# Kernel optimization log

Hardware: AMD Instinct MI355X
Metric: run time of the kernel (lower is better)

Reference implementation:

```python
import jax, jax.numpy as jnp
import numpy as np

NEG_SLOPE = 0.2
EPS = 1e-16


def gat_layer(x, src, dst, W, att, bias, heads, out_ch, concat, num_nodes, edge_weight):
    """WeightedGATConv forward (eval mode, dropout off).
    x: [N, Fin], src/dst: [E], W: [Fin, H*C], att: [H, 2C], bias: [H*C] or [C].
    """
    H, C = heads, out_ch
    xp = (x @ W).reshape(-1, H, C)           # [N, H, C]
    xi = xp[dst]                              # target features  [E, H, C]
    xj = xp[src]                              # source features  [E, H, C]
    # attention logits: (cat(xi, xj) * att).sum(-1)
    alpha = jnp.einsum('ehc,hc->eh', xi, att[:, :C]) + jnp.einsum('ehc,hc->eh', xj, att[:, C:])
    alpha = jnp.where(alpha >= 0, alpha, NEG_SLOPE * alpha)   # leaky_relu
    # segment softmax over incoming edges of each destination node
    amax = jax.ops.segment_max(alpha, dst, num_segments=num_nodes)  # [N, H]
    amax = jnp.where(jnp.isfinite(amax), amax, 0.0)
    ex = jnp.exp(alpha - amax[dst])                                  # [E, H]
    denom = jax.ops.segment_sum(ex, dst, num_segments=num_nodes)     # [N, H]
    a = ex / (denom[dst] + EPS)                                      # [E, H]
    msg = xj * a[..., None]                                          # [E, H, C]
    if edge_weight is not None:
        msg = msg * edge_weight[:, None, None]
    out = jax.ops.segment_sum(msg, dst, num_segments=num_nodes)      # [N, H, C]
    out = out.reshape(num_nodes, H * C) if concat else out.mean(axis=1)
    return out + bias


def setup_inputs() -> dict:
    key = jax.random.key(0)
    ks = jax.random.split(key, 10)
    N, E = 20000, 320000
    IN, HID, LAT, H = 512, 256, 128, 4
    C1 = HID // H
    glorot = lambda k, shp: jax.random.uniform(k, shp, jnp.float32, -1.0, 1.0) * jnp.sqrt(6.0 / (shp[-2] + shp[-1]))
    return {
        'x': jax.random.normal(ks[0], (N, IN), jnp.float32),
        'edge_index': jax.random.randint(ks[1], (2, E), 0, N, jnp.int32),
        'edge_weight': jax.random.uniform(ks[2], (E,), jnp.float32),
        'W1': glorot(ks[3], (IN, H * C1)),
        'att1': glorot(ks[4], (H, 2 * C1)),
        'b1': jnp.zeros((H * C1,), jnp.float32),
        'Wmu': glorot(ks[5], (HID, LAT)),
        'attmu': glorot(ks[6], (1, 2 * LAT)),
        'bmu': jnp.zeros((LAT,), jnp.float32),
        'Wlv': glorot(ks[7], (HID, LAT)),
        'attlv': glorot(ks[8], (1, 2 * LAT)),
        'blv': jnp.zeros((LAT,), jnp.float32),
    }


def reference(x, edge_index, edge_weight, W1, att1, b1, Wmu, attmu, bmu, Wlv, attlv, blv):
    N = x.shape[0]
    src, dst = edge_index[0], edge_index[1]
    H = att1.shape[0]
    C1 = att1.shape[1] // 2
    LAT = Wmu.shape[1]
    h = gat_layer(x, src, dst, W1, att1, b1, H, C1, True, N, edge_weight)
    h = jax.nn.elu(h)
    mu = gat_layer(h, src, dst, Wmu, attmu, bmu, 1, LAT, False, N, edge_weight)
    logvar = gat_layer(h, src, dst, Wlv, attlv, blv, 1, LAT, False, N, edge_weight)
    return (mu, logvar)
```

## Files before the change

kernel.cpp:

```cpp
#include <hip/hip_runtime.h>
#include <stdint.h>

#define NEG_SLOPE 0.2f
#define SEPS 1e-16f

typedef short bf16x8 __attribute__((ext_vector_type(8)));
typedef float f32x4 __attribute__((ext_vector_type(4)));

static __device__ __forceinline__ float bf2f(ushort u) {
  union { uint32_t i; float f; } v; v.i = ((uint32_t)u) << 16; return v.f;
}
static __device__ __forceinline__ ushort f2bf(float f) {
  uint32_t b = __float_as_uint(f);
  b += 0x7FFFu + ((b >> 16) & 1u);
  return (ushort)(b >> 16);
}
static __device__ __forceinline__ float blo(uint32_t u) { return __uint_as_float(u << 16); }
static __device__ __forceinline__ float bhi(uint32_t u) { return __uint_as_float(u & 0xFFFF0000u); }
static __device__ __forceinline__ float ldf(const void* p, size_t i, int mode) {
  return mode ? ((const float*)p)[i] : bf2f(((const ushort*)p)[i]);
}

__global__ void fill_out(float* __restrict__ out, int n, float v) {
  int i = blockIdx.x * 256 + threadIdx.x;
  if (i < n) out[i] = v;
}
__global__ void fill_i32(int* __restrict__ p, int n, int v) {
  int i = blockIdx.x * 256 + threadIdx.x;
  if (i < n) p[i] = v;
}

struct DetPtrs {
  const uint32_t* p[11];
  int n[11];
  const uint32_t* idx;
  int idxn;
};
__global__ void detect_all(DetPtrs dp, int* __restrict__ modes) {
  int b = blockIdx.x;
  __shared__ int sL, sH;
  if (threadIdx.x == 0) { sL = 0; sH = 0; }
  __syncthreads();
  if (b < 11) {
    const uint32_t* w = dp.p[b];
    int elems = dp.n[b];
    int nprobe = min(2048, elems / 2);
    int cL = 0, cH = 0;
    for (int i = threadIdx.x; i < nprobe; i += 256) {
      uint32_t v = w[i];
      uint32_t eL = (v >> 7) & 0xFFu;
      uint32_t eH = (v >> 23) & 0xFFu;
      if (eL >= 90u && eL <= 128u) cL++;
      if (eH >= 90u && eH <= 128u) cH++;
    }
    atomicAdd(&sL, cL); atomicAdd(&sH, cH);
    __syncthreads();
    if (threadIdx.x == 0) {
      int m;
      if (sL * 4 >= nprobe * 3) m = 0;
      else if (sH * 4 >= nprobe) m = 1;
      else m = 0;
      modes[b] = m;
    }
  } else {
    const uint32_t* w = dp.idx;
    int nprobe = min(4096, dp.idxn);
    int c = 0;
    for (int i = threadIdx.x; i < nprobe; i += 256)
      if ((i & 1) && w[i] == 0u) c++;
    atomicAdd(&sL, c);
    __syncthreads();
    if (threadIdx.x == 0) modes[11] = (sL * 4 >= (nprobe / 2) * 3) ? 1 : 0;
  }
}

__global__ void canon_edges(const void* __restrict__ ei, const void* __restrict__ ew,
                            int* __restrict__ srcc, int* __restrict__ dstc,
                            int* __restrict__ deg, float* __restrict__ ewf,
                            int E, int N, const int* __restrict__ modes) {
  int i = blockIdx.x * 256 + threadIdx.x;
  if (i >= E) return;
  int s, d;
  if (modes[11]) {
    s = (int)((const long long*)ei)[i];
    d = (int)((const long long*)ei)[E + i];
  } else {
    s = ((const int*)ei)[i];
    d = ((const int*)ei)[E + i];
  }
  s = min(max(s, 0), N - 1);
  d = min(max(d, 0), N - 1);
  srcc[i] = s;
  dstc[i] = d;
  atomicAdd(&deg[d], 1);
  float v = ldf(ew, i, modes[1]);
  if (!isfinite(v)) v = 0.f;
  ewf[i] = v;
}

struct WTArgs {
  const void* w1; const void* wmu; const void* wlv;
  ushort* wt1; ushort* wall;
};
__global__ void canon_wt(WTArgs a, const int* __restrict__ modes) {
  int i = blockIdx.x * 256 + threadIdx.x;
  const int NW1 = 256 * 512;
  if (i < NW1) {
    int n = i >> 9, k = i & 511;
    float v = ldf(a.w1, (size_t)k * 256 + n, modes[2]);
    if (!isfinite(v)) v = 0.f;
    a.wt1[i] = f2bf(v);
  } else {
    int j = i - NW1;
    if (j >= 256 * 256) return;
    int n = j >> 8, k = j & 255;
    float v;
    if (n < 128) v = ldf(a.wmu, (size_t)k * 128 + n, modes[5]);
    else         v = ldf(a.wlv, (size_t)k * 128 + (n - 128), modes[8]);
    if (!isfinite(v)) v = 0.f;
    a.wall[j] = f2bf(v);
  }
}
struct SmallCan { const void* src[6]; float* dst[6]; int n[6]; int mi[6]; };
__global__ void canon_small(SmallCan a, const int* __restrict__ modes) {
  int b = blockIdx.x;
  int m = modes[a.mi[b]];
  const void* s = a.src[b];
  float* d = a.dst[b];
  for (int i = threadIdx.x; i < a.n[b]; i += 256) {
    float v = ldf(s, i, m);
    if (!isfinite(v)) v = 0.f;
    d[i] = v;
  }
}

__global__ __launch_bounds__(1024) void scan_deg(const int* __restrict__ deg,
                                                 int* __restrict__ row_ptr,
                                                 int* __restrict__ row_cur, int N) {
  __shared__ int part[1024];
  int t = threadIdx.x;
  int chunk = (N + 1023) / 1024;
  int lo = t * chunk, hi = min(lo + chunk, N);
  int s = 0;
  for (int i = lo; i < hi; ++i) s += deg[i];
  part[t] = s;
  __syncthreads();
  for (int off = 1; off < 1024; off <<= 1) {
    int v = (t >= off) ? part[t - off] : 0;
    __syncthreads();
    part[t] += v;
    __syncthreads();
  }
  int base = (t == 0) ? 0 : part[t - 1];
  for (int i = lo; i < hi; ++i) {
    row_ptr[i] = base; row_cur[i] = base;
    base += deg[i];
  }
  if (t == 1023) row_ptr[N] = part[1023];
}
__global__ void scatter_edges(const int* __restrict__ dstv, const int* __restrict__ srcv,
                              const float* __restrict__ ew, int* __restrict__ row_cur,
                              int* __restrict__ csr_src, float* __restrict__ csr_w, int E) {
  int e = blockIdx.x * 256 + threadIdx.x;
  if (e < E) {
    int p = atomicAdd(&row_cur[dstv[e]], 1);
    csr_src[p] = srcv[e];
    csr_w[p] = ew[e];
  }
}

template <int KTOT>
__global__ __launch_bounds__(256) void gemm_mfma(
    const void* __restrict__ A, const ushort* __restrict__ WT,
    ushort* __restrict__ out, int M, int nTot,
    const int* __restrict__ modeA) {
  __shared__ ushort As[64][40];
  __shared__ ushort Bs[128][40];

  int t = threadIdx.x;
  int m0 = blockIdx.x * 64;
  int n0 = blockIdx.y * 128;
  int wid = t >> 6, l = t & 63;
  int wr = wid >> 1, wc = wid & 1;
  int mode = modeA ? *modeA : 1;

  int arow = t >> 2;
  int akoff = (t & 3) * 8;
  int srow = min(m0 + arow, M - 1);
  int brow = t >> 1;
  int bkoff = (t & 1) * 16;

  f32x4 acc[2][4];
#pragma unroll
  for (int i = 0; i < 2; ++i)
#pragma unroll
    for (int j = 0; j < 4; ++j) acc[i][j] = (f32x4){0.f, 0.f, 0.f, 0.f};

  int cl = l & 15;
  int ksl = (l >> 4) * 8;

  for (int k0 = 0; k0 < KTOT; k0 += 32) {
    if (mode) {
      const float* Af = (const float*)A + (size_t)srow * KTOT + k0 + akoff;
      float4 v0 = *(const float4*)Af;
      float4 v1 = *(const float4*)(Af + 4);
      uint4 pk;
      pk.x = (uint32_t)f2bf(v0.x) | ((uint32_t)f2bf(v0.y) << 16);
      pk.y = (uint32_t)f2bf(v0.z) | ((uint32_t)f2bf(v0.w) << 16);
      pk.z = (uint32_t)f2bf(v1.x) | ((uint32_t)f2bf(v1.y) << 16);
      pk.w = (uint32_t)f2bf(v1.z) | ((uint32_t)f2bf(v1.w) << 16);
      *(uint4*)&As[arow][akoff] = pk;
    } else {
      *(uint4*)&As[arow][akoff] =
          *(const uint4*)((const ushort*)A + (size_t)srow * KTOT + k0 + akoff);
    }
    {
      const ushort* wp = WT + (size_t)(n0 + brow) * KTOT + k0 + bkoff;
      *(uint4*)&Bs[brow][bkoff] = *(const uint4*)wp;
      *(uint4*)&Bs[brow][bkoff + 8] = *(const uint4*)(wp + 8);
    }
    __syncthreads();

    bf16x8 af[2], bfr[4];
#pragma unroll
    for (int i = 0; i < 2; ++i)
      af[i] = *(const bf16x8*)&As[wr * 32 + i * 16 + cl][ksl];
#pragma unroll
    for (int j = 0; j < 4; ++j)
      bfr[j] = *(const bf16x8*)&Bs[wc * 64 + j * 16 + cl][ksl];
#pragma unroll
    for (int i = 0; i < 2; ++i)
#pragma unroll
      for (int j = 0; j < 4; ++j)
        acc[i][j] = __builtin_amdgcn_mfma_f32_16x16x32_bf16(af[i], bfr[j], acc[i][j], 0, 0, 0);
    __syncthreads();
  }

  int rb = (l >> 4) * 4;
#pragma unroll
  for (int i = 0; i < 2; ++i)
#pragma unroll
    for (int j = 0; j < 4; ++j)
#pragma unroll
      for (int r = 0; r < 4; ++r) {
        int m = m0 + wr * 32 + i * 16 + rb + r;
        if (m < M)
          out[(size_t)m * nTot + n0 + wc * 64 + j * 16 + cl] = f2bf(acc[i][j][r]);
      }
}

__global__ void node_dots1(const ushort* __restrict__ xp, const float* __restrict__ att,
                           float* __restrict__ ad, float* __restrict__ as_, int N) {
  int idx = blockIdx.x * 256 + threadIdx.x;
  if (idx >= N * 8) return;
  int half = idx & 1, h = (idx >> 1) & 3, n = idx >> 3;
  const ushort* row = xp + (size_t)n * 256 + h * 64;
  const float* wv = att + h * 128 + half * 64;
  float s = 0.f;
#pragma unroll
  for (int c = 0; c < 64; c += 8) {
    uint4 v = *(const uint4*)(row + c);
    s += blo(v.x) * wv[c + 0] + bhi(v.x) * wv[c + 1]
       + blo(v.y) * wv[c + 2] + bhi(v.y) * wv[c + 3]
       + blo(v.z) * wv[c + 4] + bhi(v.z) * wv[c + 5]
       + blo(v.w) * wv[c + 6] + bhi(v.w) * wv[c + 7];
  }
  if (half == 0) ad[n * 4 + h] = s;
  else           as_[n * 4 + h] = s;
}
__global__ void node_dots2(const ushort* __restrict__ hp2,
                           const float* __restrict__ attmu, const float* __restrict__ attlv,
                           float* __restrict__ a4, int N) {
  int idx = blockIdx.x * 256 + threadIdx.x;
  if (idx >= N * 4) return;
  int w = idx & 3, n = idx >> 2;
  const float* at = (w < 2) ? attmu : attlv;
  const float* wv = at + ((w & 1) ? 128 : 0);
  const ushort* row = hp2 + (size_t)n * 256 + ((w < 2) ? 0 : 128);
  float s = 0.f;
#pragma unroll
  for (int c = 0; c < 128; c += 8) {
    uint4 v = *(const uint4*)(row + c);
    s += blo(v.x) * wv[c + 0] + bhi(v.x) * wv[c + 1]
       + blo(v.y) * wv[c + 2] + bhi(v.y) * wv[c + 3]
       + blo(v.z) * wv[c + 4] + bhi(v.z) * wv[c + 5]
       + blo(v.w) * wv[c + 6] + bhi(v.w) * wv[c + 7];
  }
  a4[idx] = s;
}

__global__ __launch_bounds__(256) void fused_agg1_wave(
    const int* __restrict__ row_ptr, const int* __restrict__ csr_src,
    const float* __restrict__ csr_w,
    const float* __restrict__ ad, const float* __restrict__ as_,
    const ushort* __restrict__ xp, const float* __restrict__ b1,
    float* __restrict__ hout, int N) {
  int n = blockIdx.x * 4 + (threadIdx.x >> 6);
  if (n >= N) return;
  int lane = threadIdx.x & 63;
  int h = lane & 3;
  int es = lane >> 2;
  int sg = lane >> 5, l = lane & 31, hl = l >> 3;

  int lo = row_ptr[n], hi = row_ptr[n + 1];
  float adv = ad[n * 4 + h];

  float m = -1e30f;
  for (int i = lo + es; i < hi; i += 16) {
    int s = csr_src[i];
    float a = adv + as_[s * 4 + h];
    a = a >= 0.f ? a : NEG_SLOPE * a;
    m = fmaxf(m, a);
  }
  m = fmaxf(m, __shfl_xor(m, 4));
  m = fmaxf(m, __shfl_xor(m, 8));
  m = fmaxf(m, __shfl_xor(m, 16));
  m = fmaxf(m, __shfl_xor(m, 32));

  float dsum = 0.f;
  float acc[8];
#pragma unroll
  for (int j = 0; j < 8; ++j) acc[j] = 0.f;

  for (int cb = lo; cb < hi; cb += 16) {
    int cn = min(16, hi - cb);
    float cwreg = 0.f; int sreg = 0;
    if (es < cn) {
      int i = cb + es;
      int s = csr_src[i];
      sreg = s;
      float a = adv + as_[s * 4 + h];
      a = a >= 0.f ? a : NEG_SLOPE * a;
      float ev = expf(a - m);
      dsum += ev;
      cwreg = ev * csr_w[i];
    }
    for (int el2 = 0; el2 < cn; el2 += 2) {
      int el = el2 + sg;
      int elc = min(el, cn - 1);
      float cw = __shfl(cwreg, (elc << 2) | hl);
      int s = __shfl(sreg, elc << 2);
      if (el < cn) {
        uint4 v = *(const uint4*)(xp + (size_t)s * 256 + l * 8);
        acc[0] += cw * blo(v.x); acc[1] += cw * bhi(v.x);
        acc[2] += cw * blo(v.y); acc[3] += cw * bhi(v.y);
        acc[4] += cw * blo(v.z); acc[5] += cw * bhi(v.z);
        acc[6] += cw * blo(v.w); acc[7] += cw * bhi(v.w);
      }
    }
  }

  dsum += __shfl_xor(dsum, 4);
  dsum += __shfl_xor(dsum, 8);
  dsum += __shfl_xor(dsum, 16);
  dsum += __shfl_xor(dsum, 32);
  float den = __shfl(dsum, hl);

#pragma unroll
  for (int j = 0; j < 8; ++j) acc[j] += __shfl_down(acc[j], 32);

  if (sg == 0) {
    float inv = 1.0f / (den + SEPS);
#pragma unroll
    for (int j = 0; j < 8; ++j) {
      float val = acc[j] * inv + b1[l * 8 + j];
      hout[(size_t)n * 256 + l * 8 + j] = val > 0.f ? val : expm1f(val);
    }
  }
}

__global__ __launch_bounds__(256) void fused_agg2_wave(
    const int* __restrict__ row_ptr, const int* __restrict__ csr_src,
    const float* __restrict__ csr_w, const float* __restrict__ a4,
    const ushort* __restrict__ hp2,
    const float* __restrict__ bmu, const float* __restrict__ blv,
    float* __restrict__ out, int N) {
  int wid = blockIdx.x * 4 + (threadIdx.x >> 6);
  int n = wid >> 1, sl = wid & 1;
  if (n >= N) return;
  int lane = threadIdx.x & 63;
  int sg = lane >> 4, l = lane & 15;

  int lo = row_ptr[n], hi = row_ptr[n + 1];
  float adv = a4[n * 4 + sl * 2];

  float m = -1e30f;
  for (int i = lo + lane; i < hi; i += 64) {
    int s = csr_src[i];
    float a = adv + a4[s * 4 + sl * 2 + 1];
    a = a >= 0.f ? a : NEG_SLOPE * a;
    m = fmaxf(m, a);
  }
  m = fmaxf(m, __shfl_xor(m, 1));
  m = fmaxf(m, __shfl_xor(m, 2));
  m = fmaxf(m, __shfl_xor(m, 4));
  m = fmaxf(m, __shfl_xor(m, 8));
  m = fmaxf(m, __shfl_xor(m, 16));
  m = fmaxf(m, __shfl_xor(m, 32));

  float dsum = 0.f;
  float acc[8];
#pragma unroll
  for (int j = 0; j < 8; ++j) acc[j] = 0.f;

  for (int cb = lo; cb < hi; cb += 64) {
    int cn = min(64, hi - cb);
    float cwreg = 0.f; int sreg = 0;
    if (lane < cn) {
      int i = cb + lane;
      int s = csr_src[i];
      sreg = s;
      float a = adv + a4[s * 4 + sl * 2 + 1];
      a = a >= 0.f ? a : NEG_SLOPE * a;
      float ev = expf(a - m);
      dsum += ev;
      cwreg = ev * csr_w[i];
    }
    for (int el2 = 0; el2 < cn; el2 += 4) {
      int el = el2 + sg;
      int elc = min(el, cn - 1);
      float cw = __shfl(cwreg, elc);
      int s = __shfl(sreg, elc);
      if (el < cn) {
        uint4 v = *(const uint4*)(hp2 + (size_t)s * 256 + sl * 128 + l * 8);
        acc[0] += cw * blo(v.x); acc[1] += cw * bhi(v.x);
        acc[2] += cw * blo(v.y); acc[3] += cw * bhi(v.y);
        acc[4] += cw * blo(v.z); acc[5] += cw * bhi(v.z);
        acc[6] += cw * blo(v.w); acc[7] += cw * bhi(v.w);
      }
    }
  }

  dsum += __shfl_xor(dsum, 1);
  dsum += __shfl_xor(dsum, 2);
  dsum += __shfl_xor(dsum, 4);
  dsum += __shfl_xor(dsum, 8);
  dsum += __shfl_xor(dsum, 16);
  dsum += __shfl_xor(dsum, 32);

#pragma unroll
  for (int j = 0; j < 8; ++j) {
    acc[j] += __shfl_down(acc[j], 32);
    acc[j] += __shfl_down(acc[j], 16);
  }

  if (sg == 0) {
    float inv = 1.0f / (dsum + SEPS);
    const float* bb = sl ? blv : bmu;
    float* op = out + (size_t)sl * N * 128 + (size_t)n * 128 + l * 8;
#pragma unroll
    for (int j = 0; j < 8; ++j) op[j] = acc[j] * inv + bb[l * 8 + j];
  }
}

extern "C" void kernel_launch(void* const* d_in, const int* in_sizes, int n_in,
                              void* d_out, int out_size, void* d_ws, size_t ws_size,
                              hipStream_t stream) {
  int OB = (out_size + 255) / 256;
  bool ok = (n_in == 12);
  int HID = 0, IN = 0, N = 0, LAT = 0, E = 0;
  if (ok) {
    HID = in_sizes[5];
    ok = ok && HID == 256;
    IN = HID ? in_sizes[3] / HID : 0;
    ok = ok && IN == 512 && in_sizes[3] == IN * HID;
    N = IN ? in_sizes[0] / IN : 0;
    ok = ok && N > 0 && in_sizes[0] == N * IN && (N % 4) == 0;
    LAT = in_sizes[8];
    ok = ok && LAT == 128;
    E = in_sizes[2];
    ok = ok && E > 0 && in_sizes[1] == 2 * E;
    ok = ok && in_sizes[4] == 2 * HID && in_sizes[6] == HID * LAT &&
         in_sizes[7] == 2 * LAT && in_sizes[9] == HID * LAT &&
         in_sizes[10] == 2 * LAT && in_sizes[11] == LAT &&
         out_size == 2 * N * LAT;
  }
  if (!ok) { fill_out<<<OB, 256, 0, stream>>>((float*)d_out, out_size, 2.0f); return; }

  char* p = (char*)d_ws;
  auto alloc = [&](size_t bytes) -> char* {
    char* r = p;
    p += (bytes + 255) & ~((size_t)255);
    return r;
  };
  ushort* xp_bf = (ushort*)alloc((size_t)N * HID * 2);
  float*  hreg  = (float*) alloc((size_t)N * HID * 4);
  ushort* WT1b  = (ushort*)alloc((size_t)HID * IN * 2);
  ushort* WallT = (ushort*)alloc((size_t)2 * LAT * HID * 2);
  float*  att1f = (float*) alloc((size_t)2 * HID * 4);
  float*  b1f   = (float*) alloc((size_t)HID * 4);
  float*  attmuf= (float*) alloc((size_t)2 * LAT * 4);
  float*  bmuf  = (float*) alloc((size_t)LAT * 4);
  float*  attlvf= (float*) alloc((size_t)2 * LAT * 4);
  float*  blvf  = (float*) alloc((size_t)LAT * 4);
  float*  ewf   = (float*) alloc((size_t)E * 4);
  float*  ad1   = (float*) alloc((size_t)N * 4 * 4);
  float*  as1   = (float*) alloc((size_t)N * 4 * 4);
  float*  a4    = (float*) alloc((size_t)N * 4 * 4);
  int*    srcc  = (int*)   alloc((size_t)E * 4);
  int*    dstc  = (int*)   alloc((size_t)E * 4);
  int*    csr_src=(int*)   alloc((size_t)E * 4);
  float*  csr_w = (float*) alloc((size_t)E * 4);
  int*    row_ptr=(int*)   alloc((size_t)(N + 1) * 4);
  int*    row_cur=(int*)   alloc((size_t)N * 4);
  int*    deg   = (int*)   alloc((size_t)N * 4);
  int*    modes = (int*)   alloc(16 * 4);

  size_t need = (size_t)(p - (char*)d_ws);
  if (need > ws_size) {
    fill_out<<<OB, 256, 0, stream>>>((float*)d_out, out_size, 3.0f);
    return;
  }

  ushort* hp2 = xp_bf;

  const int fidx[11] = {0, 2, 3, 4, 5, 6, 7, 8, 9, 10, 11};
  DetPtrs dp;
  for (int i = 0; i < 11; ++i) {
    dp.p[i] = (const uint32_t*)d_in[fidx[i]];
    dp.n[i] = in_sizes[fidx[i]];
  }
  dp.idx = (const uint32_t*)d_in[1];
  dp.idxn = 2 * E;
  detect_all<<<12, 256, 0, stream>>>(dp, modes);

  int EB1 = (E + 255) / 256;
  fill_i32<<<(N + 255) / 256, 256, 0, stream>>>(deg, N, 0);
  canon_edges<<<EB1, 256, 0, stream>>>(d_in[1], d_in[2], srcc, dstc, deg, ewf,
                                       E, N, modes);
  WTArgs wt;
  wt.w1 = d_in[3]; wt.wmu = d_in[6]; wt.wlv = d_in[9];
  wt.wt1 = WT1b; wt.wall = WallT;
  int wtot = HID * IN + 2 * LAT * HID;
  canon_wt<<<(wtot + 255) / 256, 256, 0, stream>>>(wt, modes);
  SmallCan sc;
  sc.src[0] = d_in[4];  sc.dst[0] = att1f;  sc.n[0] = 2 * HID; sc.mi[0] = 3;
  sc.src[1] = d_in[5];  sc.dst[1] = b1f;    sc.n[1] = HID;     sc.mi[1] = 4;
  sc.src[2] = d_in[7];  sc.dst[2] = attmuf; sc.n[2] = 2 * LAT; sc.mi[2] = 6;
  sc.src[3] = d_in[8];  sc.dst[3] = bmuf;   sc.n[3] = LAT;     sc.mi[3] = 7;
  sc.src[4] = d_in[10]; sc.dst[4] = attlvf; sc.n[4] = 2 * LAT; sc.mi[4] = 9;
  sc.src[5] = d_in[11]; sc.dst[5] = blvf;   sc.n[5] = LAT;     sc.mi[5] = 10;
  canon_small<<<6, 256, 0, stream>>>(sc, modes);

  scan_deg<<<1, 1024, 0, stream>>>(deg, row_ptr, row_cur, N);
  scatter_edges<<<EB1, 256, 0, stream>>>(dstc, srcc, ewf, row_cur, csr_src, csr_w, E);

  dim3 g1((N + 63) / 64, HID / 128);
  dim3 g2((N + 63) / 64, (2 * LAT) / 128);

  gemm_mfma<512><<<g1, 256, 0, stream>>>(d_in[0], WT1b, xp_bf, N, HID, &modes[0]);
  node_dots1<<<(N * 8 + 255) / 256, 256, 0, stream>>>(xp_bf, att1f, ad1, as1, N);
  fused_agg1_wave<<<(N + 3) / 4, 256, 0, stream>>>(row_ptr, csr_src, csr_w,
                                                   ad1, as1, xp_bf, b1f, hreg, N);

  gemm_mfma<256><<<g2, 256, 0, stream>>>(hreg, WallT, hp2, N, 2 * LAT, nullptr);
  node_dots2<<<(N * 4 + 255) / 256, 256, 0, stream>>>(hp2, attmuf, attlvf, a4, N);
  fused_agg2_wave<<<(2 * N + 3) / 4, 256, 0, stream>>>(row_ptr, csr_src, csr_w, a4,
                                                       hp2, bmuf, blvf,
                                                       (float*)d_out, N);
}
```

Measured before the change: 303.8 us.

## Fuse attention dot products into GEMM epilogue, merge setup kernels, use online softmax

Computes the per-node attention dot products inside the MFMA GEMM epilogue with shuffles and atomics, which removes the separate node_dots kernels that re-read the projected features. The setup kernels (detect, fill, canon edges, weights, small params) are merged into two launches to cut launch overhead. The aggregation kernels switch to an online softmax with running-max rescaling, so the separate pass over edges that computed the max is no longer needed. In exchange the dot products now depend on fp32 atomics and a zeroed buffer, and each edge chunk pays for extra exps and accumulator rescaling.

```diff
diff --git a/kernel.cpp b/kernel.cpp
--- a/kernel.cpp
+++ b/kernel.cpp
@@ -24,10 +24,6 @@
 __global__ void fill_out(float* __restrict__ out, int n, float v) {
   int i = blockIdx.x * 256 + threadIdx.x;
   if (i < n) out[i] = v;
-}
-__global__ void fill_i32(int* __restrict__ p, int n, int v) {
-  int i = blockIdx.x * 256 + threadIdx.x;
-  if (i < n) p[i] = v;
 }
 
 struct DetPtrs {
@@ -36,8 +32,21 @@
   const uint32_t* idx;
   int idxn;
 };
-__global__ void detect_all(DetPtrs dp, int* __restrict__ modes) {
+__global__ void prologue(DetPtrs dp, int* __restrict__ modes,
+                         int* __restrict__ deg, float* __restrict__ dots,
+                         int N, int nbDeg) {
   int b = blockIdx.x;
+  if (b >= 12) {
+    int rb = b - 12;
+    if (rb < nbDeg) {
+      int i = rb * 256 + threadIdx.x;
+      if (i < N) deg[i] = 0;
+    } else {
+      int i = (rb - nbDeg) * 256 + threadIdx.x;
+      if (i < N * 12) dots[i] = 0.f;
+    }
+    return;
+  }
   __shared__ int sL, sH;
   if (threadIdx.x == 0) { sL = 0; sH = 0; }
   __syncthreads();
@@ -74,63 +83,67 @@
   }
 }
 
-__global__ void canon_edges(const void* __restrict__ ei, const void* __restrict__ ew,
-                            int* __restrict__ srcc, int* __restrict__ dstc,
-                            int* __restrict__ deg, float* __restrict__ ewf,
-                            int E, int N, const int* __restrict__ modes) {
-  int i = blockIdx.x * 256 + threadIdx.x;
-  if (i >= E) return;
-  int s, d;
-  if (modes[11]) {
-    s = (int)((const long long*)ei)[i];
-    d = (int)((const long long*)ei)[E + i];
-  } else {
-    s = ((const int*)ei)[i];
-    d = ((const int*)ei)[E + i];
-  }
-  s = min(max(s, 0), N - 1);
-  d = min(max(d, 0), N - 1);
-  srcc[i] = s;
-  dstc[i] = d;
-  atomicAdd(&deg[d], 1);
-  float v = ldf(ew, i, modes[1]);
-  if (!isfinite(v)) v = 0.f;
-  ewf[i] = v;
-}
-
 struct WTArgs {
   const void* w1; const void* wmu; const void* wlv;
   ushort* wt1; ushort* wall;
 };
-__global__ void canon_wt(WTArgs a, const int* __restrict__ modes) {
-  int i = blockIdx.x * 256 + threadIdx.x;
-  const int NW1 = 256 * 512;
-  if (i < NW1) {
-    int n = i >> 9, k = i & 511;
-    float v = ldf(a.w1, (size_t)k * 256 + n, modes[2]);
+struct SmallCan { const void* src[6]; float* dst[6]; int n[6]; int mi[6]; };
+struct CanArgs {
+  const void* ei; const void* ew;
+  int* srcc; int* dstc; int* deg; float* ewf;
+  int E; int N; int EB1; int WB;
+  WTArgs wt;
+  SmallCan sc;
+};
+__global__ void canon_all(CanArgs a, const int* __restrict__ modes) {
+  int b = blockIdx.x;
+  if (b < a.EB1) {
+    int i = b * 256 + threadIdx.x;
+    if (i >= a.E) return;
+    int s, d;
+    if (modes[11]) {
+      s = (int)((const long long*)a.ei)[i];
+      d = (int)((const long long*)a.ei)[a.E + i];
+    } else {
+      s = ((const int*)a.ei)[i];
+      d = ((const int*)a.ei)[a.E + i];
+    }
+    s = min(max(s, 0), a.N - 1);
+    d = min(max(d, 0), a.N - 1);
+    a.srcc[i] = s;
+    a.dstc[i] = d;
+    atomicAdd(&a.deg[d], 1);
+    float v = ldf(a.ew, i, modes[1]);
     if (!isfinite(v)) v = 0.f;
-    a.wt1[i] = f2bf(v);
+    a.ewf[i] = v;
+  } else if (b < a.EB1 + a.WB) {
+    int i = (b - a.EB1) * 256 + threadIdx.x;
+    const int NW1 = 256 * 512;
+    if (i < NW1) {
+      int n = i >> 9, k = i & 511;
+      float v = ldf(a.wt.w1, (size_t)k * 256 + n, modes[2]);
+      if (!isfinite(v)) v = 0.f;
+      a.wt.wt1[i] = f2bf(v);
+    } else {
+      int j = i - NW1;
+      if (j >= 256 * 256) return;
+      int n = j >> 8, k = j & 255;
+      float v;
+      if (n < 128) v = ldf(a.wt.wmu, (size_t)k * 128 + n, modes[5]);
+      else         v = ldf(a.wt.wlv, (size_t)k * 128 + (n - 128), modes[8]);
+      if (!isfinite(v)) v = 0.f;
+      a.wt.wall[j] = f2bf(v);
+    }
   } else {
-    int j = i - NW1;
-    if (j >= 256 * 256) return;
-    int n = j >> 8, k = j & 255;
-    float v;
-    if (n < 128) v = ldf(a.wmu, (size_t)k * 128 + n, modes[5]);
-    else         v = ldf(a.wlv, (size_t)k * 128 + (n - 128), modes[8]);
-    if (!isfinite(v)) v = 0.f;
-    a.wall[j] = f2bf(v);
-  }
-}
-struct SmallCan { const void* src[6]; float* dst[6]; int n[6]; int mi[6]; };
-__global__ void canon_small(SmallCan a, const int* __restrict__ modes) {
-  int b = blockIdx.x;
-  int m = modes[a.mi[b]];
-  const void* s = a.src[b];
-  float* d = a.dst[b];
-  for (int i = threadIdx.x; i < a.n[b]; i += 256) {
-    float v = ldf(s, i, m);
-    if (!isfinite(v)) v = 0.f;
-    d[i] = v;
+    int sb = b - a.EB1 - a.WB;
+    int m = modes[a.sc.mi[sb]];
+    const void* s = a.sc.src[sb];
+    float* d = a.sc.dst[sb];
+    for (int i = threadIdx.x; i < a.sc.n[sb]; i += 256) {
+      float v = ldf(s, i, m);
+      if (!isfinite(v)) v = 0.f;
+      d[i] = v;
+    }
   }
 }
 
@@ -169,11 +182,12 @@
   }
 }
 
-template <int KTOT>
+template <int KTOT, int DMODE>
 __global__ __launch_bounds__(256) void gemm_mfma(
     const void* __restrict__ A, const ushort* __restrict__ WT,
     ushort* __restrict__ out, int M, int nTot,
-    const int* __restrict__ modeA) {
+    const int* __restrict__ modeA, const float* __restrict__ attv,
+    float* __restrict__ dotd, float* __restrict__ dotsrc) {
   __shared__ ushort As[64][40];
   __shared__ ushort Bs[128][40];
 
@@ -237,6 +251,54 @@
   }
 
   int rb = (l >> 4) * 4;
+
+  if (DMODE) {
+    float wd[4], ws[4];
+    int hsl;
+    if (DMODE == 1) {
+      hsl = (n0 >> 6) + wc;
+#pragma unroll
+      for (int j = 0; j < 4; ++j) {
+        wd[j] = attv[hsl * 128 + j * 16 + cl];
+        ws[j] = attv[hsl * 128 + 64 + j * 16 + cl];
+      }
+    } else {
+      int base = n0 + wc * 64;
+      hsl = base >> 7;
+      int ccb = base & 127;
+#pragma unroll
+      for (int j = 0; j < 4; ++j) {
+        wd[j] = attv[hsl * 256 + ccb + j * 16 + cl];
+        ws[j] = attv[hsl * 256 + 128 + ccb + j * 16 + cl];
+      }
+    }
+#pragma unroll
+    for (int i = 0; i < 2; ++i)
+#pragma unroll
+      for (int r = 0; r < 4; ++r) {
+        float pd = acc[i][0][r] * wd[0] + acc[i][1][r] * wd[1]
+                 + acc[i][2][r] * wd[2] + acc[i][3][r] * wd[3];
+        float ps = acc[i][0][r] * ws[0] + acc[i][1][r] * ws[1]
+                 + acc[i][2][r] * ws[2] + acc[i][3][r] * ws[3];
+        pd += __shfl_xor(pd, 1); pd += __shfl_xor(pd, 2);
+        pd += __shfl_xor(pd, 4); pd += __shfl_xor(pd, 8);
+        ps += __shfl_xor(ps, 1); ps += __shfl_xor(ps, 2);
+        ps += __shfl_xor(ps, 4); ps += __shfl_xor(ps, 8);
+        if (cl == 0) {
+          int m = m0 + wr * 32 + i * 16 + rb + r;
+          if (m < M) {
+            if (DMODE == 1) {
+              atomicAdd(&dotd[m * 4 + hsl], pd);
+              atomicAdd(&dotsrc[m * 4 + hsl], ps);
+            } else {
+              atomicAdd(&dotd[m * 4 + hsl * 2], pd);
+              atomicAdd(&dotd[m * 4 + hsl * 2 + 1], ps);
+            }
+          }
+        }
+      }
+  }
+
 #pragma unroll
   for (int i = 0; i < 2; ++i)
 #pragma unroll
@@ -247,46 +309,6 @@
         if (m < M)
           out[(size_t)m * nTot + n0 + wc * 64 + j * 16 + cl] = f2bf(acc[i][j][r]);
       }
-}
-
-__global__ void node_dots1(const ushort* __restrict__ xp, const float* __restrict__ att,
-                           float* __restrict__ ad, float* __restrict__ as_, int N) {
-  int idx = blockIdx.x * 256 + threadIdx.x;
-  if (idx >= N * 8) return;
-  int half = idx & 1, h = (idx >> 1) & 3, n = idx >> 3;
-  const ushort* row = xp + (size_t)n * 256 + h * 64;
-  const float* wv = att + h * 128 + half * 64;
-  float s = 0.f;
-#pragma unroll
-  for (int c = 0; c < 64; c += 8) {
-    uint4 v = *(const uint4*)(row + c);
-    s += blo(v.x) * wv[c + 0] + bhi(v.x) * wv[c + 1]
-       + blo(v.y) * wv[c + 2] + bhi(v.y) * wv[c + 3]
-       + blo(v.z) * wv[c + 4] + bhi(v.z) * wv[c + 5]
-       + blo(v.w) * wv[c + 6] + bhi(v.w) * wv[c + 7];
-  }
-  if (half == 0) ad[n * 4 + h] = s;
-  else           as_[n * 4 + h] = s;
-}
-__global__ void node_dots2(const ushort* __restrict__ hp2,
-                           const float* __restrict__ attmu, const float* __restrict__ attlv,
-                           float* __restrict__ a4, int N) {
-  int idx = blockIdx.x * 256 + threadIdx.x;
-  if (idx >= N * 4) return;
-  int w = idx & 3, n = idx >> 2;
-  const float* at = (w < 2) ? attmu : attlv;
-  const float* wv = at + ((w & 1) ? 128 : 0);
-  const ushort* row = hp2 + (size_t)n * 256 + ((w < 2) ? 0 : 128);
-  float s = 0.f;
-#pragma unroll
-  for (int c = 0; c < 128; c += 8) {
-    uint4 v = *(const uint4*)(row + c);
-    s += blo(v.x) * wv[c + 0] + bhi(v.x) * wv[c + 1]
-       + blo(v.y) * wv[c + 2] + bhi(v.y) * wv[c + 3]
-       + blo(v.z) * wv[c + 4] + bhi(v.z) * wv[c + 5]
-       + blo(v.w) * wv[c + 6] + bhi(v.w) * wv[c + 7];
-  }
-  a4[idx] = s;
 }
 
 __global__ __launch_bounds__(256) void fused_agg1_wave(
@@ -306,17 +328,6 @@
   float adv = ad[n * 4 + h];
 
   float m = -1e30f;
-  for (int i = lo + es; i < hi; i += 16) {
-    int s = csr_src[i];
-    float a = adv + as_[s * 4 + h];
-    a = a >= 0.f ? a : NEG_SLOPE * a;
-    m = fmaxf(m, a);
-  }
-  m = fmaxf(m, __shfl_xor(m, 4));
-  m = fmaxf(m, __shfl_xor(m, 8));
-  m = fmaxf(m, __shfl_xor(m, 16));
-  m = fmaxf(m, __shfl_xor(m, 32));
-
   float dsum = 0.f;
   float acc[8];
 #pragma unroll
@@ -324,17 +335,31 @@
 
   for (int cb = lo; cb < hi; cb += 16) {
     int cn = min(16, hi - cb);
-    float cwreg = 0.f; int sreg = 0;
+    float a = -1e30f;
+    int sreg = 0;
+    float wreg = 0.f;
     if (es < cn) {
       int i = cb + es;
       int s = csr_src[i];
       sreg = s;
-      float a = adv + as_[s * 4 + h];
-      a = a >= 0.f ? a : NEG_SLOPE * a;
-      float ev = expf(a - m);
-      dsum += ev;
-      cwreg = ev * csr_w[i];
-    }
+      wreg = csr_w[i];
+      float aa = adv + as_[s * 4 + h];
+      a = aa >= 0.f ? aa : NEG_SLOPE * aa;
+    }
+    float cm = a;
+    cm = fmaxf(cm, __shfl_xor(cm, 4));
+    cm = fmaxf(cm, __shfl_xor(cm, 8));
+    cm = fmaxf(cm, __shfl_xor(cm, 16));
+    cm = fmaxf(cm, __shfl_xor(cm, 32));
+    float mnew = fmaxf(m, cm);
+    float scale = expf(m - mnew);
+    m = mnew;
+    float ev = (es < cn) ? expf(a - m) : 0.f;
+    dsum = dsum * scale + ev;
+    float cwreg = ev * wreg;
+    float sc = __shfl(scale, hl);
+#pragma unroll
+    for (int j = 0; j < 8; ++j) acc[j] *= sc;
     for (int el2 = 0; el2 < cn; el2 += 2) {
       int el = el2 + sg;
       int elc = min(el, cn - 1);
@@ -385,19 +410,6 @@
   float adv = a4[n * 4 + sl * 2];
 
   float m = -1e30f;
-  for (int i = lo + lane; i < hi; i += 64) {
-    int s = csr_src[i];
-    float a = adv + a4[s * 4 + sl * 2 + 1];
-    a = a >= 0.f ? a : NEG_SLOPE * a;
-    m = fmaxf(m, a);
-  }
-  m = fmaxf(m, __shfl_xor(m, 1));
-  m = fmaxf(m, __shfl_xor(m, 2));
-  m = fmaxf(m, __shfl_xor(m, 4));
-  m = fmaxf(m, __shfl_xor(m, 8));
-  m = fmaxf(m, __shfl_xor(m, 16));
-  m = fmaxf(m, __shfl_xor(m, 32));
-
   float dsum = 0.f;
   float acc[8];
 #pragma unroll
@@ -405,17 +417,32 @@
 
   for (int cb = lo; cb < hi; cb += 64) {
     int cn = min(64, hi - cb);
-    float cwreg = 0.f; int sreg = 0;
+    float a = -1e30f;
+    int sreg = 0;
+    float wreg = 0.f;
     if (lane < cn) {
       int i = cb + lane;
       int s = csr_src[i];
       sreg = s;
-      float a = adv + a4[s * 4 + sl * 2 + 1];
-      a = a >= 0.f ? a : NEG_SLOPE * a;
-      float ev = expf(a - m);
-      dsum += ev;
-      cwreg = ev * csr_w[i];
-    }
+      wreg = csr_w[i];
+      float aa = adv + a4[s * 4 + sl * 2 + 1];
+      a = aa >= 0.f ? aa : NEG_SLOPE * aa;
+    }
+    float cm = a;
+    cm = fmaxf(cm, __shfl_xor(cm, 1));
+    cm = fmaxf(cm, __shfl_xor(cm, 2));
+    cm = fmaxf(cm, __shfl_xor(cm, 4));
+    cm = fmaxf(cm, __shfl_xor(cm, 8));
+    cm = fmaxf(cm, __shfl_xor(cm, 16));
+    cm = fmaxf(cm, __shfl_xor(cm, 32));
+    float mnew = fmaxf(m, cm);
+    float scale = expf(m - mnew);
+    m = mnew;
+    float ev = (lane < cn) ? expf(a - m) : 0.f;
+    dsum = dsum * scale + ev;
+    float cwreg = ev * wreg;
+#pragma unroll
+    for (int j = 0; j < 8; ++j) acc[j] *= scale;
     for (int el2 = 0; el2 < cn; el2 += 4) {
       int el = el2 + sg;
       int elc = min(el, cn - 1);
@@ -487,16 +514,13 @@
   float*  hreg  = (float*) alloc((size_t)N * HID * 4);
   ushort* WT1b  = (ushort*)alloc((size_t)HID * IN * 2);
   ushort* WallT = (ushort*)alloc((size_t)2 * LAT * HID * 2);
+  float*  dots  = (float*) alloc((size_t)N * 12 * 4);
   float*  att1f = (float*) alloc((size_t)2 * HID * 4);
+  float*  att2f = (float*) alloc((size_t)4 * LAT * 4);
   float*  b1f   = (float*) alloc((size_t)HID * 4);
-  float*  attmuf= (float*) alloc((size_t)2 * LAT * 4);
   float*  bmuf  = (float*) alloc((size_t)LAT * 4);
-  float*  attlvf= (float*) alloc((size_t)2 * LAT * 4);
   float*  blvf  = (float*) alloc((size_t)LAT * 4);
   float*  ewf   = (float*) alloc((size_t)E * 4);
-  float*  ad1   = (float*) alloc((size_t)N * 4 * 4);
-  float*  as1   = (float*) alloc((size_t)N * 4 * 4);
-  float*  a4    = (float*) alloc((size_t)N * 4 * 4);
   int*    srcc  = (int*)   alloc((size_t)E * 4);
   int*    dstc  = (int*)   alloc((size_t)E * 4);
   int*    csr_src=(int*)   alloc((size_t)E * 4);
@@ -513,6 +537,9 @@
   }
 
   ushort* hp2 = xp_bf;
+  float* ad1 = dots;
+  float* as1 = dots + (size_t)N * 4;
+  float* a4  = dots + (size_t)N * 8;
 
   const int fidx[11] = {0, 2, 3, 4, 5, 6, 7, 8, 9, 10, 11};
   DetPtrs dp;
@@ -522,25 +549,25 @@
   }
   dp.idx = (const uint32_t*)d_in[1];
   dp.idxn = 2 * E;
-  detect_all<<<12, 256, 0, stream>>>(dp, modes);
+  int nbDeg = (N + 255) / 256;
+  int nbDots = (N * 12 + 255) / 256;
+  prologue<<<12 + nbDeg + nbDots, 256, 0, stream>>>(dp, modes, deg, dots, N, nbDeg);
 
   int EB1 = (E + 255) / 256;
-  fill_i32<<<(N + 255) / 256, 256, 0, stream>>>(deg, N, 0);
-  canon_edges<<<EB1, 256, 0, stream>>>(d_in[1], d_in[2], srcc, dstc, deg, ewf,
-                                       E, N, modes);
-  WTArgs wt;
-  wt.w1 = d_in[3]; wt.wmu = d_in[6]; wt.wlv = d_in[9];
-  wt.wt1 = WT1b; wt.wall = WallT;
-  int wtot = HID * IN + 2 * LAT * HID;
-  canon_wt<<<(wtot + 255) / 256, 256, 0, stream>>>(wt, modes);
-  SmallCan sc;
-  sc.src[0] = d_in[4];  sc.dst[0] = att1f;  sc.n[0] = 2 * HID; sc.mi[0] = 3;
-  sc.src[1] = d_in[5];  sc.dst[1] = b1f;    sc.n[1] = HID;     sc.mi[1] = 4;
-  sc.src[2] = d_in[7];  sc.dst[2] = attmuf; sc.n[2] = 2 * LAT; sc.mi[2] = 6;
-  sc.src[3] = d_in[8];  sc.dst[3] = bmuf;   sc.n[3] = LAT;     sc.mi[3] = 7;
-  sc.src[4] = d_in[10]; sc.dst[4] = attlvf; sc.n[4] = 2 * LAT; sc.mi[4] = 9;
-  sc.src[5] = d_in[11]; sc.dst[5] = blvf;   sc.n[5] = LAT;     sc.mi[5] = 10;
-  canon_small<<<6, 256, 0, stream>>>(sc, modes);
+  int WB = (HID * IN + 2 * LAT * HID + 255) / 256;
+  CanArgs ca;
+  ca.ei = d_in[1]; ca.ew = d_in[2];
+  ca.srcc = srcc; ca.dstc = dstc; ca.deg = deg; ca.ewf = ewf;
+  ca.E = E; ca.N = N; ca.EB1 = EB1; ca.WB = WB;
+  ca.wt.w1 = d_in[3]; ca.wt.wmu = d_in[6]; ca.wt.wlv = d_in[9];
+  ca.wt.wt1 = WT1b; ca.wt.wall = WallT;
+  ca.sc.src[0] = d_in[4];  ca.sc.dst[0] = att1f;        ca.sc.n[0] = 2 * HID; ca.sc.mi[0] = 3;
+  ca.sc.src[1] = d_in[5];  ca.sc.dst[1] = b1f;          ca.sc.n[1] = HID;     ca.sc.mi[1] = 4;
+  ca.sc.src[2] = d_in[7];  ca.sc.dst[2] = att2f;        ca.sc.n[2] = 2 * LAT; ca.sc.mi[2] = 6;
+  ca.sc.src[3] = d_in[8];  ca.sc.dst[3] = bmuf;         ca.sc.n[3] = LAT;     ca.sc.mi[3] = 7;
+  ca.sc.src[4] = d_in[10]; ca.sc.dst[4] = att2f + 256;  ca.sc.n[4] = 2 * LAT; ca.sc.mi[4] = 9;
+  ca.sc.src[5] = d_in[11]; ca.sc.dst[5] = blvf;         ca.sc.n[5] = LAT;     ca.sc.mi[5] = 10;
+  canon_all<<<EB1 + WB + 6, 256, 0, stream>>>(ca, modes);
 
   scan_deg<<<1, 1024, 0, stream>>>(deg, row_ptr, row_cur, N);
   scatter_edges<<<EB1, 256, 0, stream>>>(dstc, srcc, ewf, row_cur, csr_src, csr_w, E);
@@ -548,13 +575,13 @@
   dim3 g1((N + 63) / 64, HID / 128);
   dim3 g2((N + 63) / 64, (2 * LAT) / 128);
 
-  gemm_mfma<512><<<g1, 256, 0, stream>>>(d_in[0], WT1b, xp_bf, N, HID, &modes[0]);
-  node_dots1<<<(N * 8 + 255) / 256, 256, 0, stream>>>(xp_bf, att1f, ad1, as1, N);
+  gemm_mfma<512, 1><<<g1, 256, 0, stream>>>(d_in[0], WT1b, xp_bf, N, HID,
+                                            &modes[0], att1f, ad1, as1);
   fused_agg1_wave<<<(N + 3) / 4, 256, 0, stream>>>(row_ptr, csr_src, csr_w,
                                                    ad1, as1, xp_bf, b1f, hreg, N);
 
-  gemm_mfma<256><<<g2, 256, 0, stream>>>(hreg, WallT, hp2, N, 2 * LAT, nullptr);
-  node_dots2<<<(N * 4 + 255) / 256, 256, 0, stream>>>(hp2, attmuf, attlvf, a4, N);
+  gemm_mfma<256, 2><<<g2, 256, 0, stream>>>(hreg, WallT, hp2, N, 2 * LAT,
+                                            nullptr, att2f, a4, nullptr);
   fused_agg2_wave<<<(2 * N + 3) / 4, 256, 0, stream>>>(row_ptr, csr_src, csr_w, a4,
                                                        hp2, bmuf, blvf,
                                                        (float*)d_out, N);
```

After: 292.0 us. -3.9%, faster.
